# Kernel optimization log

Measured on AMD Instinct MI355X. Metric: run time of the kernel, lower is better.

The kernel has to match this reference:

```python
import jax, jax.numpy as jnp
import numpy as np

NUM_HEADS = 4
EMBED_DIM = 256
HEAD_DIM = EMBED_DIM // NUM_HEADS
B, N = 4, 4096


def setup_inputs() -> dict:
    key = jax.random.key(0)
    kq, kk, kv, kw = jax.random.split(key, 4)
    q = jax.random.normal(kq, (B, N, EMBED_DIM), dtype=jnp.float32)
    k = jax.random.normal(kk, (B, N, EMBED_DIM), dtype=jnp.float32)
    v = jax.random.normal(kv, (B, N, EMBED_DIM), dtype=jnp.float32)
    W_out = jax.random.normal(kw, (EMBED_DIM, EMBED_DIM), dtype=jnp.float32) * (1.0 / np.sqrt(EMBED_DIM))
    b_out = jnp.zeros((EMBED_DIM,), dtype=jnp.float32)
    return {"q": q, "k": k, "v": v, "W_out": W_out, "b_out": b_out}


def reference(q, k, v, W_out, b_out):
    b, n, _ = q.shape
    # [b, n, e] -> [b, h, n, d]
    qh = q.reshape(b, n, NUM_HEADS, HEAD_DIM).transpose(0, 2, 1, 3)
    kh = k.reshape(b, n, NUM_HEADS, HEAD_DIM).transpose(0, 2, 1, 3)
    vh = v.reshape(b, n, NUM_HEADS, HEAD_DIM).transpose(0, 2, 1, 3)
    scale = 1.0 / jnp.sqrt(jnp.asarray(HEAD_DIM, dtype=qh.dtype))
    # full [b, h, n, n] score matrix, as in the original module
    attn = jnp.einsum('bhqd,bhkd->bhqk', qh, kh) * scale
    attn = jax.nn.softmax(attn, axis=-1)
    out = jnp.einsum('bhqk,bhkd->bhqd', attn, vh)
    out = out.transpose(0, 2, 1, 3).reshape(b, n, EMBED_DIM)
    # nn.Linear: x @ W.T + b
    return out @ W_out.T + b_out
```

## Files before the change

kernel.cpp:

```cpp
#include <hip/hip_runtime.h>
#include <hip/hip_bf16.h>

#define B_ 4
#define H_ 4
#define N_ 4096
#define D_ 64
#define E_ 256
#define KVB 64
#define QBLK 128
#define NT (N_ / KVB)

typedef short short8 __attribute__((ext_vector_type(8)));
typedef float f32x4 __attribute__((ext_vector_type(4)));
typedef float f32x16 __attribute__((ext_vector_type(16)));

__device__ __forceinline__ ushort f2bf(float f) {
  union { float f; unsigned u; } a; a.f = f;
  unsigned r = a.u + 0x7fffu + ((a.u >> 16) & 1u);
  return (ushort)(r >> 16);
}

__device__ __forceinline__ uint4 pack8(float a0, float a1, float a2, float a3,
                                       float a4, float a5, float a6, float a7) {
  uint4 u;
  u.x = (unsigned)f2bf(a0) | ((unsigned)f2bf(a1) << 16);
  u.y = (unsigned)f2bf(a2) | ((unsigned)f2bf(a3) << 16);
  u.z = (unsigned)f2bf(a4) | ((unsigned)f2bf(a5) << 16);
  u.w = (unsigned)f2bf(a6) | ((unsigned)f2bf(a7) << 16);
  return u;
}

__device__ __forceinline__ unsigned cvt_pk_bf16(float lo, float hi) {
  unsigned r;
  asm("v_cvt_pk_bf16_f32 %0, %1, %2" : "=v"(r) : "v"(lo), "v"(hi));
  return r;
}

__device__ __forceinline__ void permlane32_swap(unsigned &a, unsigned &b) {
  asm volatile("v_permlane32_swap_b32 %0, %1" : "+v"(a), "+v"(b));
}

__global__ void cast_w_kernel(const float* __restrict__ W, ushort* __restrict__ Wb) {
  int i = blockIdx.x * blockDim.x + threadIdx.x;
  float4 x = ((const float4*)W)[i];
  ushort4 o;
  o.x = f2bf(x.x); o.y = f2bf(x.y); o.z = f2bf(x.z); o.w = f2bf(x.w);
  ((ushort4*)Wb)[i] = o;
}

__global__ void prep_kv(const float* __restrict__ k, const float* __restrict__ v,
                        ushort* __restrict__ Kb, ushort* __restrict__ Vtb) {
  __shared__ float vt[64][65];
  const int gid = blockIdx.x;
  const int bh = gid >> 6, t = gid & 63;
  const int b = bh >> 2, h = bh & 3;
  const int tid = threadIdx.x;
  const int rr = tid >> 4, cc = (tid & 15) * 4;
  const float* kg = k + ((size_t)b * N_ + t * 64) * E_ + h * 64;
  const float* vg = v + ((size_t)b * N_ + t * 64) * E_ + h * 64;
  ushort* ko = Kb + (size_t)gid * 4096;
  ushort* vo = Vtb + (size_t)gid * 4096;

  for (int it = 0; it < 4; ++it) {
    int r = rr + it * 16;
    float4 vx = *(const float4*)(vg + (size_t)r * E_ + cc);
    vt[r][cc] = vx.x; vt[r][cc + 1] = vx.y; vt[r][cc + 2] = vx.z; vt[r][cc + 3] = vx.w;
  }
  __syncthreads();

  for (int j = 0; j < 2; ++j) {
    int u = j * 256 + tid;
    int frag = u >> 6, l = u & 63;
    int a = (frag >> 2) * 32 + (l & 31);
    int c0 = (frag & 3) * 16 + ((l >> 5) & 1) * 8;
    {
      const float* p = kg + (size_t)a * E_ + c0;
      float4 x0 = *(const float4*)(p);
      float4 x1 = *(const float4*)(p + 4);
      *(uint4*)(ko + u * 8) = pack8(x0.x, x0.y, x0.z, x0.w, x1.x, x1.y, x1.z, x1.w);
    }
    {
      *(uint4*)(vo + u * 8) = pack8(vt[c0][a], vt[c0 + 1][a], vt[c0 + 2][a], vt[c0 + 3][a],
                                    vt[c0 + 4][a], vt[c0 + 5][a], vt[c0 + 6][a], vt[c0 + 7][a]);
    }
  }
}

__launch_bounds__(256, 2)
__global__ void attn_kernel(const float* __restrict__ q,
                            const ushort* __restrict__ Kb,
                            const ushort* __restrict__ Vtb,
                            ushort* __restrict__ X) {
  __shared__ __attribute__((aligned(16))) ushort Ks[2][4096];
  __shared__ __attribute__((aligned(16))) ushort Vs[2][4096];
  __shared__ float Lb[4][32];

  const int bid = blockIdx.x;
  const int swz = (bid & 7) * 64 + (bid >> 3);
  const int bh = swz >> 5;
  const int qt = swz & 31;
  const int b = bh >> 2, h = bh & 3;
  const int tid = threadIdx.x;
  const int wid = tid >> 6;
  const int lane = tid & 63;
  const int ln = lane & 31;
  const int hi = lane >> 5;

  const char* Kg = (const char*)Kb + (size_t)bh * NT * 8192;
  const char* Vg = (const char*)Vtb + (size_t)bh * NT * 8192;

  const float SC = 0.125f * 1.44269504f;
  const int qrow0 = qt * QBLK + wid * 32;
  const float* Qg = q + ((size_t)b * N_ + qrow0 + ln) * E_ + h * D_;
  short8 qf[4];
#pragma unroll
  for (int ks = 0; ks < 4; ++ks) {
    const float* p = Qg + ks * 16 + hi * 8;
    float4 x0 = *(const float4*)(p);
    float4 x1 = *(const float4*)(p + 4);
    short8 f;
    f[0] = (short)f2bf(x0.x * SC); f[1] = (short)f2bf(x0.y * SC);
    f[2] = (short)f2bf(x0.z * SC); f[3] = (short)f2bf(x0.w * SC);
    f[4] = (short)f2bf(x1.x * SC); f[5] = (short)f2bf(x1.y * SC);
    f[6] = (short)f2bf(x1.z * SC); f[7] = (short)f2bf(x1.w * SC);
    qf[ks] = f;
  }

  f32x16 O0 = (f32x16)0.0f, O1 = (f32x16)0.0f;
  float lsum = 0.f;

  {
    uint4 k0 = *(const uint4*)(Kg + tid * 16);
    uint4 k1 = *(const uint4*)(Kg + 4096 + tid * 16);
    uint4 v0 = *(const uint4*)(Vg + tid * 16);
    uint4 v1 = *(const uint4*)(Vg + 4096 + tid * 16);
    *(uint4*)((char*)Ks[0] + tid * 16) = k0;
    *(uint4*)((char*)Ks[0] + 4096 + tid * 16) = k1;
    *(uint4*)((char*)Vs[0] + tid * 16) = v0;
    *(uint4*)((char*)Vs[0] + 4096 + tid * 16) = v1;
  }
  __syncthreads();
  int cur = 0;

  for (int t = 0; t < NT; ++t) {
    const bool pfn = (t + 1 < NT);
    uint4 rk0, rk1, rv0, rv1;
    if (pfn) {
      const char* kg = Kg + (size_t)(t + 1) * 8192;
      const char* vg = Vg + (size_t)(t + 1) * 8192;
      rk0 = *(const uint4*)(kg + tid * 16);
      rk1 = *(const uint4*)(kg + 4096 + tid * 16);
      rv0 = *(const uint4*)(vg + tid * 16);
      rv1 = *(const uint4*)(vg + 4096 + tid * 16);
    }

    short8 kf[2][4];
#pragma unroll
    for (int nb = 0; nb < 2; ++nb)
#pragma unroll
      for (int ks = 0; ks < 4; ++ks)
        kf[nb][ks] = *(short8*)((char*)Ks[cur] + (nb * 4 + ks) * 1024 + lane * 16);

    f32x16 S0 = (f32x16)0.0f, S1 = (f32x16)0.0f;
    __builtin_amdgcn_s_setprio(1);
#pragma unroll
    for (int ks = 0; ks < 4; ++ks) {
      S0 = __builtin_amdgcn_mfma_f32_32x32x16_bf16(kf[0][ks], qf[ks], S0, 0, 0, 0);
      S1 = __builtin_amdgcn_mfma_f32_32x32x16_bf16(kf[1][ks], qf[ks], S1, 0, 0, 0);
    }
    __builtin_amdgcn_s_setprio(0);

    float p[32];
#pragma unroll
    for (int i = 0; i < 16; ++i) {
      p[i]      = __builtin_amdgcn_exp2f(S0[i]);
      p[16 + i] = __builtin_amdgcn_exp2f(S1[i]);
    }
    {
      float s1[16];
#pragma unroll
      for (int i = 0; i < 16; ++i) s1[i] = p[2 * i] + p[2 * i + 1];
#pragma unroll
      for (int i = 0; i < 8; ++i) s1[i] = s1[2 * i] + s1[2 * i + 1];
#pragma unroll
      for (int i = 0; i < 4; ++i) s1[i] = s1[2 * i] + s1[2 * i + 1];
      lsum += (s1[0] + s1[1]) + (s1[2] + s1[3]);
    }

    short8 pa[4];
#pragma unroll
    for (int nb = 0; nb < 2; ++nb)
#pragma unroll
      for (int ksp = 0; ksp < 2; ++ksp) {
        int base = nb * 16 + ksp * 8;
        unsigned w0 = cvt_pk_bf16(p[base + 0], p[base + 1]);
        unsigned w2 = cvt_pk_bf16(p[base + 4], p[base + 5]);
        permlane32_swap(w0, w2);
        unsigned w1 = cvt_pk_bf16(p[base + 2], p[base + 3]);
        unsigned w3 = cvt_pk_bf16(p[base + 6], p[base + 7]);
        permlane32_swap(w1, w3);
        uint4 u; u.x = w0; u.y = w1; u.z = w2; u.w = w3;
        union { uint4 u4; short8 s8; } cv; cv.u4 = u;
        pa[nb * 2 + ksp] = cv.s8;
      }

    if (pfn) {
      *(uint4*)((char*)Ks[cur ^ 1] + tid * 16) = rk0;
      *(uint4*)((char*)Ks[cur ^ 1] + 4096 + tid * 16) = rk1;
      *(uint4*)((char*)Vs[cur ^ 1] + tid * 16) = rv0;
      *(uint4*)((char*)Vs[cur ^ 1] + 4096 + tid * 16) = rv1;
    }

    short8 vf[2][4];
#pragma unroll
    for (int db = 0; db < 2; ++db)
#pragma unroll
      for (int ks = 0; ks < 4; ++ks)
        vf[db][ks] = *(short8*)((char*)Vs[cur] + (db * 4 + ks) * 1024 + lane * 16);

    __builtin_amdgcn_s_setprio(1);
#pragma unroll
    for (int ks = 0; ks < 4; ++ks) {
      O0 = __builtin_amdgcn_mfma_f32_32x32x16_bf16(pa[ks], vf[0][ks], O0, 0, 0, 0);
      O1 = __builtin_amdgcn_mfma_f32_32x32x16_bf16(pa[ks], vf[1][ks], O1, 0, 0, 0);
    }
    __builtin_amdgcn_s_setprio(0);

    __syncthreads();
    cur ^= 1;
  }

  float l = lsum + __shfl_xor(lsum, 32);
  if (lane < 32) Lb[wid][lane] = l;
  asm volatile("" ::: "memory");
  float inv[16];
#pragma unroll
  for (int r = 0; r < 16; ++r)
    inv[r] = 1.0f / Lb[wid][(r & 3) + 8 * (r >> 2) + 4 * hi];

  ushort* Xp = X + ((size_t)b * N_) * E_ + h * D_;
#pragma unroll
  for (int r = 0; r < 16; ++r) {
    int qrow = qrow0 + (r & 3) + 8 * (r >> 2) + 4 * hi;
    Xp[(size_t)qrow * E_ + ln]      = f2bf(O0[r] * inv[r]);
    Xp[(size_t)qrow * E_ + 32 + ln] = f2bf(O1[r] * inv[r]);
  }
}

__launch_bounds__(256, 2)
__global__ void proj_kernel(const ushort* __restrict__ X, const ushort* __restrict__ Wb,
                            const float* __restrict__ bias, float* __restrict__ out) {
  const int m0   = blockIdx.x * 64;
  const int tid  = threadIdx.x;
  const int wid  = tid >> 6;
  const int lane = tid & 63;
  const int g    = lane >> 4;
  const int lr   = lane & 15;
  const int n0   = wid * 64;

  f32x4 acc[4][4];
  for (int mb = 0; mb < 4; ++mb)
    for (int nb = 0; nb < 4; ++nb)
      acc[mb][nb] = (f32x4){0.f, 0.f, 0.f, 0.f};

  for (int k0 = 0; k0 < E_; k0 += 32) {
    short8 af[4], bfr[4];
    for (int mb = 0; mb < 4; ++mb)
      af[mb] = *(const short8*)(X + (size_t)(m0 + mb * 16 + lr) * E_ + k0 + g * 8);
    for (int nb = 0; nb < 4; ++nb)
      bfr[nb] = *(const short8*)(Wb + (size_t)(n0 + nb * 16 + lr) * E_ + k0 + g * 8);
    for (int mb = 0; mb < 4; ++mb)
      for (int nb = 0; nb < 4; ++nb)
        acc[mb][nb] = __builtin_amdgcn_mfma_f32_16x16x32_bf16(af[mb], bfr[nb], acc[mb][nb], 0, 0, 0);
  }

  for (int nb = 0; nb < 4; ++nb) {
    float bv = bias[n0 + nb * 16 + lr];
    for (int mb = 0; mb < 4; ++mb)
      for (int r = 0; r < 4; ++r)
        out[(size_t)(m0 + mb * 16 + g * 4 + r) * E_ + n0 + nb * 16 + lr] = acc[mb][nb][r] + bv;
  }
}

extern "C" void kernel_launch(void* const* d_in, const int* in_sizes, int n_in,
                              void* d_out, int out_size, void* d_ws, size_t ws_size,
                              hipStream_t stream) {
  const float* q    = (const float*)d_in[0];
  const float* k    = (const float*)d_in[1];
  const float* v    = (const float*)d_in[2];
  const float* W    = (const float*)d_in[3];
  const float* bias = (const float*)d_in[4];

  char* ws = (char*)d_ws;
  ushort* X   = (ushort*)ws;
  ushort* Wb  = (ushort*)(ws + 8388608);
  ushort* Kb  = (ushort*)(ws + 8388608 + 131072);
  ushort* Vtb = (ushort*)(ws + 8388608 + 131072 + 8388608);

  cast_w_kernel<<<64, 256, 0, stream>>>(W, Wb);
  prep_kv<<<B_ * H_ * NT, 256, 0, stream>>>(k, v, Kb, Vtb);
  attn_kernel<<<B_ * H_ * (N_ / QBLK), 256, 0, stream>>>(q, Kb, Vtb, X);
  proj_kernel<<<(B_ * N_) / 64, 256, 0, stream>>>(X, Wb, bias, (float*)d_out);
}
```

Before: 111.6 us.

## Split KV range across two wave groups per block and merge partial outputs

```diff
diff --git a/kernel.cpp b/kernel.cpp
--- a/kernel.cpp
+++ b/kernel.cpp
@@ -9,6 +9,7 @@
 #define KVB 64
 #define QBLK 128
 #define NT (N_ / KVB)
+#define NR (NT / 2)
 
 typedef short short8 __attribute__((ext_vector_type(8)));
 typedef float f32x4 __attribute__((ext_vector_type(4)));
@@ -50,6 +51,7 @@
 
 __global__ void prep_kv(const float* __restrict__ k, const float* __restrict__ v,
                         ushort* __restrict__ Kb, ushort* __restrict__ Vtb) {
+  __shared__ float kt[64][65];
   __shared__ float vt[64][65];
   const int gid = blockIdx.x;
   const int bh = gid >> 6, t = gid & 63;
@@ -63,7 +65,9 @@
 
   for (int it = 0; it < 4; ++it) {
     int r = rr + it * 16;
+    float4 kx = *(const float4*)(kg + (size_t)r * E_ + cc);
     float4 vx = *(const float4*)(vg + (size_t)r * E_ + cc);
+    kt[r][cc] = kx.x; kt[r][cc + 1] = kx.y; kt[r][cc + 2] = kx.z; kt[r][cc + 3] = kx.w;
     vt[r][cc] = vx.x; vt[r][cc + 1] = vx.y; vt[r][cc + 2] = vx.z; vt[r][cc + 3] = vx.w;
   }
   __syncthreads();
@@ -73,27 +77,22 @@
     int frag = u >> 6, l = u & 63;
     int a = (frag >> 2) * 32 + (l & 31);
     int c0 = (frag & 3) * 16 + ((l >> 5) & 1) * 8;
-    {
-      const float* p = kg + (size_t)a * E_ + c0;
-      float4 x0 = *(const float4*)(p);
-      float4 x1 = *(const float4*)(p + 4);
-      *(uint4*)(ko + u * 8) = pack8(x0.x, x0.y, x0.z, x0.w, x1.x, x1.y, x1.z, x1.w);
-    }
-    {
-      *(uint4*)(vo + u * 8) = pack8(vt[c0][a], vt[c0 + 1][a], vt[c0 + 2][a], vt[c0 + 3][a],
-                                    vt[c0 + 4][a], vt[c0 + 5][a], vt[c0 + 6][a], vt[c0 + 7][a]);
-    }
-  }
-}
-
-__launch_bounds__(256, 2)
+    *(uint4*)(ko + u * 8) = pack8(kt[a][c0], kt[a][c0 + 1], kt[a][c0 + 2], kt[a][c0 + 3],
+                                  kt[a][c0 + 4], kt[a][c0 + 5], kt[a][c0 + 6], kt[a][c0 + 7]);
+    *(uint4*)(vo + u * 8) = pack8(vt[c0][a], vt[c0 + 1][a], vt[c0 + 2][a], vt[c0 + 3][a],
+                                  vt[c0 + 4][a], vt[c0 + 5][a], vt[c0 + 6][a], vt[c0 + 7][a]);
+  }
+}
+
+__launch_bounds__(512, 4)
 __global__ void attn_kernel(const float* __restrict__ q,
                             const ushort* __restrict__ Kb,
                             const ushort* __restrict__ Vtb,
                             ushort* __restrict__ X) {
-  __shared__ __attribute__((aligned(16))) ushort Ks[2][4096];
-  __shared__ __attribute__((aligned(16))) ushort Vs[2][4096];
+  __shared__ __attribute__((aligned(16))) ushort Ks[2][2][4096];
+  __shared__ __attribute__((aligned(16))) ushort Vs[2][2][4096];
   __shared__ float Lb[4][32];
+  __shared__ float Lb2[4][32];
 
   const int bid = blockIdx.x;
   const int swz = (bid & 7) * 64 + (bid >> 3);
@@ -102,6 +101,8 @@
   const int b = bh >> 2, h = bh & 3;
   const int tid = threadIdx.x;
   const int wid = tid >> 6;
+  const int wq = wid & 3;
+  const int up = wid >> 2;
   const int lane = tid & 63;
   const int ln = lane & 31;
   const int hi = lane >> 5;
@@ -110,7 +111,7 @@
   const char* Vg = (const char*)Vtb + (size_t)bh * NT * 8192;
 
   const float SC = 0.125f * 1.44269504f;
-  const int qrow0 = qt * QBLK + wid * 32;
+  const int qrow0 = qt * QBLK + wq * 32;
   const float* Qg = q + ((size_t)b * N_ + qrow0 + ln) * E_ + h * D_;
   short8 qf[4];
 #pragma unroll
@@ -131,35 +132,38 @@
 
   {
     uint4 k0 = *(const uint4*)(Kg + tid * 16);
-    uint4 k1 = *(const uint4*)(Kg + 4096 + tid * 16);
+    uint4 k1 = *(const uint4*)(Kg + 8192 + tid * 16);
     uint4 v0 = *(const uint4*)(Vg + tid * 16);
-    uint4 v1 = *(const uint4*)(Vg + 4096 + tid * 16);
-    *(uint4*)((char*)Ks[0] + tid * 16) = k0;
-    *(uint4*)((char*)Ks[0] + 4096 + tid * 16) = k1;
-    *(uint4*)((char*)Vs[0] + tid * 16) = v0;
-    *(uint4*)((char*)Vs[0] + 4096 + tid * 16) = v1;
+    uint4 v1 = *(const uint4*)(Vg + 8192 + tid * 16);
+    *(uint4*)((char*)&Ks[0][0][0] + tid * 16) = k0;
+    *(uint4*)((char*)&Ks[0][1][0] + tid * 16) = k1;
+    *(uint4*)((char*)&Vs[0][0][0] + tid * 16) = v0;
+    *(uint4*)((char*)&Vs[0][1][0] + tid * 16) = v1;
   }
   __syncthreads();
   int cur = 0;
 
-  for (int t = 0; t < NT; ++t) {
-    const bool pfn = (t + 1 < NT);
+  for (int r = 0; r < NR; ++r) {
+    const bool pfn = (r + 1 < NR);
     uint4 rk0, rk1, rv0, rv1;
     if (pfn) {
-      const char* kg = Kg + (size_t)(t + 1) * 8192;
-      const char* vg = Vg + (size_t)(t + 1) * 8192;
+      const char* kg = Kg + (size_t)(2 * r + 2) * 8192;
+      const char* vg = Vg + (size_t)(2 * r + 2) * 8192;
       rk0 = *(const uint4*)(kg + tid * 16);
-      rk1 = *(const uint4*)(kg + 4096 + tid * 16);
+      rk1 = *(const uint4*)(kg + 8192 + tid * 16);
       rv0 = *(const uint4*)(vg + tid * 16);
-      rv1 = *(const uint4*)(vg + 4096 + tid * 16);
-    }
+      rv1 = *(const uint4*)(vg + 8192 + tid * 16);
+    }
+
+    const char* Kl = (const char*)&Ks[cur][up][0];
+    const char* Vl = (const char*)&Vs[cur][up][0];
 
     short8 kf[2][4];
 #pragma unroll
     for (int nb = 0; nb < 2; ++nb)
 #pragma unroll
       for (int ks = 0; ks < 4; ++ks)
-        kf[nb][ks] = *(short8*)((char*)Ks[cur] + (nb * 4 + ks) * 1024 + lane * 16);
+        kf[nb][ks] = *(short8*)(Kl + (nb * 4 + ks) * 1024 + lane * 16);
 
     f32x16 S0 = (f32x16)0.0f, S1 = (f32x16)0.0f;
     __builtin_amdgcn_s_setprio(1);
@@ -205,10 +209,10 @@
       }
 
     if (pfn) {
-      *(uint4*)((char*)Ks[cur ^ 1] + tid * 16) = rk0;
-      *(uint4*)((char*)Ks[cur ^ 1] + 4096 + tid * 16) = rk1;
-      *(uint4*)((char*)Vs[cur ^ 1] + tid * 16) = rv0;
-      *(uint4*)((char*)Vs[cur ^ 1] + 4096 + tid * 16) = rv1;
+      *(uint4*)((char*)&Ks[cur ^ 1][0][0] + tid * 16) = rk0;
+      *(uint4*)((char*)&Ks[cur ^ 1][1][0] + tid * 16) = rk1;
+      *(uint4*)((char*)&Vs[cur ^ 1][0][0] + tid * 16) = rv0;
+      *(uint4*)((char*)&Vs[cur ^ 1][1][0] + tid * 16) = rv1;
     }
 
     short8 vf[2][4];
@@ -216,7 +220,7 @@
     for (int db = 0; db < 2; ++db)
 #pragma unroll
       for (int ks = 0; ks < 4; ++ks)
-        vf[db][ks] = *(short8*)((char*)Vs[cur] + (db * 4 + ks) * 1024 + lane * 16);
+        vf[db][ks] = *(short8*)(Vl + (db * 4 + ks) * 1024 + lane * 16);
 
     __builtin_amdgcn_s_setprio(1);
 #pragma unroll
@@ -231,19 +235,37 @@
   }
 
   float l = lsum + __shfl_xor(lsum, 32);
-  if (lane < 32) Lb[wid][lane] = l;
-  asm volatile("" ::: "memory");
-  float inv[16];
-#pragma unroll
-  for (int r = 0; r < 16; ++r)
-    inv[r] = 1.0f / Lb[wid][(r & 3) + 8 * (r >> 2) + 4 * hi];
-
-  ushort* Xp = X + ((size_t)b * N_) * E_ + h * D_;
-#pragma unroll
-  for (int r = 0; r < 16; ++r) {
-    int qrow = qrow0 + (r & 3) + 8 * (r >> 2) + 4 * hi;
-    Xp[(size_t)qrow * E_ + ln]      = f2bf(O0[r] * inv[r]);
-    Xp[(size_t)qrow * E_ + 32 + ln] = f2bf(O1[r] * inv[r]);
+  float* Ox = (float*)&Ks[0][0][0];
+  if (up) {
+    if (lane < 32) Lb[wq][ln] = l;
+#pragma unroll
+    for (int r2 = 0; r2 < 16; ++r2) {
+      Ox[wq * 1024 + r2 * 64 + lane]        = O0[r2];
+      Ox[4096 + wq * 1024 + r2 * 64 + lane] = O1[r2];
+    }
+  }
+  __syncthreads();
+  if (!up) {
+    float ltot = l + Lb[wq][ln];
+    if (lane < 32) Lb2[wq][ln] = ltot;
+    asm volatile("" ::: "memory");
+#pragma unroll
+    for (int r2 = 0; r2 < 16; ++r2) {
+      O0[r2] += Ox[wq * 1024 + r2 * 64 + lane];
+      O1[r2] += Ox[4096 + wq * 1024 + r2 * 64 + lane];
+    }
+    float inv[16];
+#pragma unroll
+    for (int r2 = 0; r2 < 16; ++r2)
+      inv[r2] = 1.0f / Lb2[wq][(r2 & 3) + 8 * (r2 >> 2) + 4 * hi];
+
+    ushort* Xp = X + ((size_t)b * N_) * E_ + h * D_;
+#pragma unroll
+    for (int r2 = 0; r2 < 16; ++r2) {
+      int qrow = qrow0 + (r2 & 3) + 8 * (r2 >> 2) + 4 * hi;
+      Xp[(size_t)qrow * E_ + ln]      = f2bf(O0[r2] * inv[r2]);
+      Xp[(size_t)qrow * E_ + 32 + ln] = f2bf(O1[r2] * inv[r2]);
+    }
   }
 }
 
@@ -299,6 +321,6 @@
 
   cast_w_kernel<<<64, 256, 0, stream>>>(W, Wb);
   prep_kv<<<B_ * H_ * NT, 256, 0, stream>>>(k, v, Kb, Vtb);
-  attn_kernel<<<B_ * H_ * (N_ / QBLK), 256, 0, stream>>>(q, Kb, Vtb, X);
+  attn_kernel<<<B_ * H_ * (N_ / QBLK), 512, 0, stream>>>(q, Kb, Vtb, X);
   proj_kernel<<<(B_ * N_) / 64, 256, 0, stream>>>(X, Wb, bias, (float*)d_out);
 }
```

After: 111.9 us. About the same (+0.2%).

## Split KV tile across wave pairs in attention and stage K through LDS in prep

Applied to the files above, without the earlier changes.

```diff
diff --git a/kernel.cpp b/kernel.cpp
--- a/kernel.cpp
+++ b/kernel.cpp
@@ -7,7 +7,7 @@
 #define D_ 64
 #define E_ 256
 #define KVB 64
-#define QBLK 128
+#define QBLK 64
 #define NT (N_ / KVB)
 
 typedef short short8 __attribute__((ext_vector_type(8)));
@@ -50,6 +50,7 @@
 
 __global__ void prep_kv(const float* __restrict__ k, const float* __restrict__ v,
                         ushort* __restrict__ Kb, ushort* __restrict__ Vtb) {
+  __shared__ float kt[64][65];
   __shared__ float vt[64][65];
   const int gid = blockIdx.x;
   const int bh = gid >> 6, t = gid & 63;
@@ -63,7 +64,9 @@
 
   for (int it = 0; it < 4; ++it) {
     int r = rr + it * 16;
+    float4 kx = *(const float4*)(kg + (size_t)r * E_ + cc);
     float4 vx = *(const float4*)(vg + (size_t)r * E_ + cc);
+    kt[r][cc] = kx.x; kt[r][cc + 1] = kx.y; kt[r][cc + 2] = kx.z; kt[r][cc + 3] = kx.w;
     vt[r][cc] = vx.x; vt[r][cc + 1] = vx.y; vt[r][cc + 2] = vx.z; vt[r][cc + 3] = vx.w;
   }
   __syncthreads();
@@ -73,35 +76,32 @@
     int frag = u >> 6, l = u & 63;
     int a = (frag >> 2) * 32 + (l & 31);
     int c0 = (frag & 3) * 16 + ((l >> 5) & 1) * 8;
-    {
-      const float* p = kg + (size_t)a * E_ + c0;
-      float4 x0 = *(const float4*)(p);
-      float4 x1 = *(const float4*)(p + 4);
-      *(uint4*)(ko + u * 8) = pack8(x0.x, x0.y, x0.z, x0.w, x1.x, x1.y, x1.z, x1.w);
-    }
-    {
-      *(uint4*)(vo + u * 8) = pack8(vt[c0][a], vt[c0 + 1][a], vt[c0 + 2][a], vt[c0 + 3][a],
-                                    vt[c0 + 4][a], vt[c0 + 5][a], vt[c0 + 6][a], vt[c0 + 7][a]);
-    }
-  }
-}
-
-__launch_bounds__(256, 2)
+    *(uint4*)(ko + u * 8) = pack8(kt[a][c0], kt[a][c0 + 1], kt[a][c0 + 2], kt[a][c0 + 3],
+                                  kt[a][c0 + 4], kt[a][c0 + 5], kt[a][c0 + 6], kt[a][c0 + 7]);
+    *(uint4*)(vo + u * 8) = pack8(vt[c0][a], vt[c0 + 1][a], vt[c0 + 2][a], vt[c0 + 3][a],
+                                  vt[c0 + 4][a], vt[c0 + 5][a], vt[c0 + 6][a], vt[c0 + 7][a]);
+  }
+}
+
+__launch_bounds__(256, 4)
 __global__ void attn_kernel(const float* __restrict__ q,
                             const ushort* __restrict__ Kb,
                             const ushort* __restrict__ Vtb,
                             ushort* __restrict__ X) {
   __shared__ __attribute__((aligned(16))) ushort Ks[2][4096];
   __shared__ __attribute__((aligned(16))) ushort Vs[2][4096];
-  __shared__ float Lb[4][32];
+  __shared__ float Lb[2][32];
+  __shared__ float Lb2[2][32];
 
   const int bid = blockIdx.x;
-  const int swz = (bid & 7) * 64 + (bid >> 3);
-  const int bh = swz >> 5;
-  const int qt = swz & 31;
+  const int swz = (bid & 7) * 128 + (bid >> 3);
+  const int bh = swz >> 6;
+  const int qt = swz & 63;
   const int b = bh >> 2, h = bh & 3;
   const int tid = threadIdx.x;
   const int wid = tid >> 6;
+  const int wq = wid & 1;
+  const int kh = wid >> 1;
   const int lane = tid & 63;
   const int ln = lane & 31;
   const int hi = lane >> 5;
@@ -110,7 +110,7 @@
   const char* Vg = (const char*)Vtb + (size_t)bh * NT * 8192;
 
   const float SC = 0.125f * 1.44269504f;
-  const int qrow0 = qt * QBLK + wid * 32;
+  const int qrow0 = qt * QBLK + wq * 32;
   const float* Qg = q + ((size_t)b * N_ + qrow0 + ln) * E_ + h * D_;
   short8 qf[4];
 #pragma unroll
@@ -154,55 +154,51 @@
       rv1 = *(const uint4*)(vg + 4096 + tid * 16);
     }
 
-    short8 kf[2][4];
-#pragma unroll
-    for (int nb = 0; nb < 2; ++nb)
-#pragma unroll
-      for (int ks = 0; ks < 4; ++ks)
-        kf[nb][ks] = *(short8*)((char*)Ks[cur] + (nb * 4 + ks) * 1024 + lane * 16);
-
-    f32x16 S0 = (f32x16)0.0f, S1 = (f32x16)0.0f;
+    short8 kf[4];
+#pragma unroll
+    for (int ks = 0; ks < 4; ++ks)
+      kf[ks] = *(short8*)((char*)Ks[cur] + (kh * 4 + ks) * 1024 + lane * 16);
+
+    f32x16 S0 = (f32x16)0.0f;
     __builtin_amdgcn_s_setprio(1);
 #pragma unroll
-    for (int ks = 0; ks < 4; ++ks) {
-      S0 = __builtin_amdgcn_mfma_f32_32x32x16_bf16(kf[0][ks], qf[ks], S0, 0, 0, 0);
-      S1 = __builtin_amdgcn_mfma_f32_32x32x16_bf16(kf[1][ks], qf[ks], S1, 0, 0, 0);
-    }
+    for (int ks = 0; ks < 4; ++ks)
+      S0 = __builtin_amdgcn_mfma_f32_32x32x16_bf16(kf[ks], qf[ks], S0, 0, 0, 0);
     __builtin_amdgcn_s_setprio(0);
 
-    float p[32];
-#pragma unroll
-    for (int i = 0; i < 16; ++i) {
-      p[i]      = __builtin_amdgcn_exp2f(S0[i]);
-      p[16 + i] = __builtin_amdgcn_exp2f(S1[i]);
-    }
+    short8 vf[2][2];
+#pragma unroll
+    for (int db = 0; db < 2; ++db)
+#pragma unroll
+      for (int s = 0; s < 2; ++s)
+        vf[db][s] = *(short8*)((char*)Vs[cur] + (db * 4 + kh * 2 + s) * 1024 + lane * 16);
+
+    float p[16];
+#pragma unroll
+    for (int i = 0; i < 16; ++i) p[i] = __builtin_amdgcn_exp2f(S0[i]);
     {
-      float s1[16];
-#pragma unroll
-      for (int i = 0; i < 16; ++i) s1[i] = p[2 * i] + p[2 * i + 1];
-#pragma unroll
-      for (int i = 0; i < 8; ++i) s1[i] = s1[2 * i] + s1[2 * i + 1];
+      float s1[8];
+#pragma unroll
+      for (int i = 0; i < 8; ++i) s1[i] = p[2 * i] + p[2 * i + 1];
 #pragma unroll
       for (int i = 0; i < 4; ++i) s1[i] = s1[2 * i] + s1[2 * i + 1];
       lsum += (s1[0] + s1[1]) + (s1[2] + s1[3]);
     }
 
-    short8 pa[4];
-#pragma unroll
-    for (int nb = 0; nb < 2; ++nb)
-#pragma unroll
-      for (int ksp = 0; ksp < 2; ++ksp) {
-        int base = nb * 16 + ksp * 8;
-        unsigned w0 = cvt_pk_bf16(p[base + 0], p[base + 1]);
-        unsigned w2 = cvt_pk_bf16(p[base + 4], p[base + 5]);
-        permlane32_swap(w0, w2);
-        unsigned w1 = cvt_pk_bf16(p[base + 2], p[base + 3]);
-        unsigned w3 = cvt_pk_bf16(p[base + 6], p[base + 7]);
-        permlane32_swap(w1, w3);
-        uint4 u; u.x = w0; u.y = w1; u.z = w2; u.w = w3;
-        union { uint4 u4; short8 s8; } cv; cv.u4 = u;
-        pa[nb * 2 + ksp] = cv.s8;
-      }
+    short8 pa[2];
+#pragma unroll
+    for (int s = 0; s < 2; ++s) {
+      int base = s * 8;
+      unsigned w0 = cvt_pk_bf16(p[base + 0], p[base + 1]);
+      unsigned w2 = cvt_pk_bf16(p[base + 4], p[base + 5]);
+      permlane32_swap(w0, w2);
+      unsigned w1 = cvt_pk_bf16(p[base + 2], p[base + 3]);
+      unsigned w3 = cvt_pk_bf16(p[base + 6], p[base + 7]);
+      permlane32_swap(w1, w3);
+      uint4 u; u.x = w0; u.y = w1; u.z = w2; u.w = w3;
+      union { uint4 u4; short8 s8; } cv; cv.u4 = u;
+      pa[s] = cv.s8;
+    }
 
     if (pfn) {
       *(uint4*)((char*)Ks[cur ^ 1] + tid * 16) = rk0;
@@ -211,18 +207,11 @@
       *(uint4*)((char*)Vs[cur ^ 1] + 4096 + tid * 16) = rv1;
     }
 
-    short8 vf[2][4];
-#pragma unroll
-    for (int db = 0; db < 2; ++db)
-#pragma unroll
-      for (int ks = 0; ks < 4; ++ks)
-        vf[db][ks] = *(short8*)((char*)Vs[cur] + (db * 4 + ks) * 1024 + lane * 16);
-
     __builtin_amdgcn_s_setprio(1);
 #pragma unroll
-    for (int ks = 0; ks < 4; ++ks) {
-      O0 = __builtin_amdgcn_mfma_f32_32x32x16_bf16(pa[ks], vf[0][ks], O0, 0, 0, 0);
-      O1 = __builtin_amdgcn_mfma_f32_32x32x16_bf16(pa[ks], vf[1][ks], O1, 0, 0, 0);
+    for (int s = 0; s < 2; ++s) {
+      O0 = __builtin_amdgcn_mfma_f32_32x32x16_bf16(pa[s], vf[0][s], O0, 0, 0, 0);
+      O1 = __builtin_amdgcn_mfma_f32_32x32x16_bf16(pa[s], vf[1][s], O1, 0, 0, 0);
     }
     __builtin_amdgcn_s_setprio(0);
 
@@ -231,19 +220,37 @@
   }
 
   float l = lsum + __shfl_xor(lsum, 32);
-  if (lane < 32) Lb[wid][lane] = l;
-  asm volatile("" ::: "memory");
-  float inv[16];
-#pragma unroll
-  for (int r = 0; r < 16; ++r)
-    inv[r] = 1.0f / Lb[wid][(r & 3) + 8 * (r >> 2) + 4 * hi];
-
-  ushort* Xp = X + ((size_t)b * N_) * E_ + h * D_;
-#pragma unroll
-  for (int r = 0; r < 16; ++r) {
-    int qrow = qrow0 + (r & 3) + 8 * (r >> 2) + 4 * hi;
-    Xp[(size_t)qrow * E_ + ln]      = f2bf(O0[r] * inv[r]);
-    Xp[(size_t)qrow * E_ + 32 + ln] = f2bf(O1[r] * inv[r]);
+  float* Ox = (float*)&Ks[0][0];
+  if (kh) {
+    if (lane < 32) Lb[wq][ln] = l;
+#pragma unroll
+    for (int r2 = 0; r2 < 16; ++r2) {
+      Ox[wq * 2048 + r2 * 64 + lane]        = O0[r2];
+      Ox[wq * 2048 + 1024 + r2 * 64 + lane] = O1[r2];
+    }
+  }
+  __syncthreads();
+  if (!kh) {
+    float ltot = l + Lb[wq][ln];
+    if (lane < 32) Lb2[wq][ln] = ltot;
+    asm volatile("" ::: "memory");
+#pragma unroll
+    for (int r2 = 0; r2 < 16; ++r2) {
+      O0[r2] += Ox[wq * 2048 + r2 * 64 + lane];
+      O1[r2] += Ox[wq * 2048 + 1024 + r2 * 64 + lane];
+    }
+    float inv[16];
+#pragma unroll
+    for (int r2 = 0; r2 < 16; ++r2)
+      inv[r2] = 1.0f / Lb2[wq][(r2 & 3) + 8 * (r2 >> 2) + 4 * hi];
+
+    ushort* Xp = X + ((size_t)b * N_) * E_ + h * D_;
+#pragma unroll
+    for (int r2 = 0; r2 < 16; ++r2) {
+      int qrow = qrow0 + (r2 & 3) + 8 * (r2 >> 2) + 4 * hi;
+      Xp[(size_t)qrow * E_ + ln]      = f2bf(O0[r2] * inv[r2]);
+      Xp[(size_t)qrow * E_ + 32 + ln] = f2bf(O1[r2] * inv[r2]);
+    }
   }
 }
 
```

Result: slower. 118.2 us (+5.9%).
